# Performance work log

Hardware: AMD Instinct MI355X
Metric: run time of the kernel (lower is better)

The kernel has to match this reference:

```python
import jax, jax.numpy as jnp
import numpy as np

NUM_BRANCHES = 3
NUM_LAYERS = 4
HIDDEN = 256
IN_DIM = 128
NUM_GRAPHS = 256
NUM_CLASSES = 10
TOPK_RATIO = 0.5
GATE_INIT = 0.8


def matrix_neighbors(branch, layer, num_branches):
    nbrs = []
    if layer > 0:
        nbrs.append((branch, layer - 1))
    for other in (branch - 1, branch + 1):
        if 0 <= other < num_branches:
            nbrs.append((other, layer))
    if layer > 0:
        for other in (branch - 1, branch + 1):
            if 0 <= other < num_branches:
                nbrs.append((other, layer - 1))
    return nbrs


def topk_mask(t, ratio):
    d = t.shape[-1]
    k = max(1, min(d, int(np.ceil(d * ratio))))
    if k >= d:
        return jnp.ones_like(t)
    _, idx = jax.lax.top_k(jnp.abs(t), k)
    rows = jnp.arange(t.shape[0])[:, None]
    return jnp.zeros_like(t).at[rows, idx].set(1.0)


def setup_inputs():
    key = jax.random.key(0)
    ks = jax.random.split(key, 10)
    n, e = 50000, 800000
    x = jax.random.normal(ks[0], (n, IN_DIM), dtype=jnp.float32)
    edge_index = jax.random.randint(ks[1], (2, e), 0, n)
    batch = jnp.sort(jax.random.randint(ks[2], (n,), 0, NUM_GRAPHS))
    s = 0.05
    Win = jax.random.normal(ks[3], (NUM_BRANCHES, IN_DIM, HIDDEN), dtype=jnp.float32) * s
    b_in = jnp.zeros((NUM_BRANCHES, HIDDEN), dtype=jnp.float32)
    Whid = jax.random.normal(ks[4], (NUM_LAYERS - 1, NUM_BRANCHES, HIDDEN, HIDDEN), dtype=jnp.float32) * s
    bhid = jnp.zeros((NUM_LAYERS - 1, NUM_BRANCHES, HIDDEN), dtype=jnp.float32)
    gate_logit = jnp.asarray(np.log(GATE_INIT / (1.0 - GATE_INIT)), dtype=jnp.float32)
    Wc = jax.random.normal(ks[5], (HIDDEN, NUM_CLASSES), dtype=jnp.float32) * s
    bc = jnp.zeros((NUM_CLASSES,), dtype=jnp.float32)
    return {"x": x, "edge_index": edge_index, "batch": batch, "Win": Win,
            "b_in": b_in, "Whid": Whid, "bhid": bhid, "gate_logit": gate_logit,
            "Wc": Wc, "bc": bc}


def _forward(x, edge_index, batch, Win, b_in, Whid, bhid, gate_logit, Wc, bc):
    n = x.shape[0]
    loops = jnp.arange(n)
    row = jnp.concatenate([edge_index[0], loops])  # source
    col = jnp.concatenate([edge_index[1], loops])  # target
    deg = jax.ops.segment_sum(jnp.ones_like(col, dtype=x.dtype), col, num_segments=n)
    dinv = jnp.where(deg > 0, jax.lax.rsqrt(deg), 0.0)
    norm = dinv[row] * dinv[col]  # [E+N]

    def gcn(h, W, b):
        hw = h @ W  # [n, H]
        agg = jax.ops.segment_sum(hw[row] * norm[:, None], col, num_segments=n)
        return agg + b

    gate = jax.nn.sigmoid(gate_logit)
    states = [x for _ in range(NUM_BRANCHES)]
    for layer in range(NUM_LAYERS):
        props = []
        for b in range(NUM_BRANCHES):
            if layer == 0:
                p = gcn(states[b], Win[b], b_in[b])
            else:
                p = gcn(states[b], Whid[layer - 1, b], bhid[layer - 1, b])
            props.append(jax.nn.relu(p))
        new_states = []
        for b in range(NUM_BRANCHES):
            fused = props[b]
            nbrs = matrix_neighbors(b, layer, NUM_BRANCHES)
            if nbrs:
                rs = jnp.zeros_like(fused)
                for (sb, sl) in nbrs:
                    src = props[sb] if sl == layer else states[sb]
                    rs = rs + src * topk_mask(src, TOPK_RATIO)
                fused = fused + gate * rs
            new_states.append(jax.nn.relu(fused))  # dropout is identity in eval
        states = new_states

    counts = jax.ops.segment_sum(jnp.ones((n,), dtype=x.dtype), batch, num_segments=NUM_GRAPHS)
    denom = jnp.maximum(counts, 1.0)[:, None]
    embs = [jax.ops.segment_sum(s, batch, num_segments=NUM_GRAPHS) / denom for s in states]
    final = jnp.mean(jnp.stack(embs, axis=0), axis=0)  # [G, H]
    logits = final @ Wc + bc
    return logits, final


def reference(x, edge_index, batch, Win, b_in, Whid, bhid, gate_logit, Wc, bc):
    return _forward(x, edge_index, batch, Win, b_in, Whid, bhid, gate_logit, Wc, bc)
```

## Files before the change

kernel.cpp:

```cpp
#include <hip/hip_runtime.h>
#include <hip/hip_fp16.h>

#define NB 3
#define HIDDEN 256
#define INDIM 128
#define NGRAPH 256
#define NCLS 10
#define NMAX 50048
#define EMAX 800000

typedef unsigned short u16;
typedef unsigned long long ull;
typedef _Float16 f16_t;
typedef f16_t f16x8 __attribute__((ext_vector_type(8)));
typedef float f32x4 __attribute__((ext_vector_type(4)));

__device__ __align__(16) u16   g_states[(size_t)NMAX * NB * HIDDEN];
__device__ __align__(16) u16   g_props [(size_t)NMAX * NB * HIDDEN];
__device__ __align__(16) u16   g_agg3 [(size_t)NMAX * NB * HIDDEN];
__device__ __align__(16) u16   g_xh    [(size_t)NMAX * INDIM];
__device__ __align__(16) u16   g_whin [(size_t)NB * INDIM * HIDDEN];
__device__ __align__(16) u16   g_whid [(size_t)9 * HIDDEN * HIDDEN];
__device__ float g_fin   [NGRAPH * HIDDEN];
__device__ float g_dinv  [NMAX];
__device__ float g_ewts  [EMAX];
__device__ int   g_rowptr[NMAX + 1];
__device__ int   g_cidx  [EMAX];
__device__ int   g_cnt   [NMAX];
__device__ int   g_gs    [NGRAPH];
__device__ int   g_gc    [NGRAPH];

union HU { u16 u; __half h; };
__device__ __forceinline__ float h2f(u16 v) { HU x; x.u = v; return __half2float(x.h); }
__device__ __forceinline__ u16 f2h(float f) { HU x; x.h = __float2half_rn(f); return x.u; }
__device__ __forceinline__ float relu_f(float x) { return x > 0.f ? x : 0.f; }

__device__ __forceinline__ void fma8(float* acc, uint4 v, float w) {
    unsigned uu[4] = {v.x, v.y, v.z, v.w};
    #pragma unroll
    for (int q = 0; q < 4; ++q) {
        HU lo, hi; lo.u = (u16)(uu[q] & 0xFFFFu); hi.u = (u16)(uu[q] >> 16);
        acc[q * 2 + 0] += w * __half2float(lo.h);
        acc[q * 2 + 1] += w * __half2float(hi.h);
    }
}

__global__ void zero_cnt_k(int n) {
    int i = blockIdx.x * 256 + threadIdx.x;
    if (i < n) g_cnt[i] = 0;
}
__global__ void zero_gk() {
    int i = threadIdx.x;
    g_gs[i] = 0; g_gc[i] = 0;
}
__global__ void cvt_xh_k(const float* __restrict__ x, int cnt) {
    int i = blockIdx.x * 256 + threadIdx.x;
    if (i < cnt) g_xh[i] = f2h(x[i]);
}
__global__ void cvt_wt_k(const float* __restrict__ src, int which, int K, int total) {
    int i = blockIdx.x * 256 + threadIdx.x;
    if (i >= total) return;
    int kc = K * 256;
    int b = i / kc; int rem = i - b * kc;
    int k = rem >> 8; int c = rem & 255;
    u16* dst = which ? g_whid : g_whin;
    dst[(size_t)b * kc + (size_t)c * K + k] = f2h(src[i]);
}

__global__ void count_edges_k(const int* __restrict__ col, int E) {
    int i = blockIdx.x * 256 + threadIdx.x;
    if (i < E) atomicAdd(&g_cnt[col[i]], 1);
}
__global__ void dinv_k(int n) {
    int i = blockIdx.x * 256 + threadIdx.x;
    if (i < n) g_dinv[i] = rsqrtf((float)(g_cnt[i] + 1));
}
__global__ __launch_bounds__(1024) void scan_k(int n) {
    __shared__ int sm[1024];
    __shared__ int carry_s;
    int t = threadIdx.x;
    if (t == 0) carry_s = 0;
    __syncthreads();
    for (int base = 0; base < n; base += 1024) {
        int i = base + t;
        int v = (i < n) ? g_cnt[i] : 0;
        sm[t] = v;
        __syncthreads();
        for (int off = 1; off < 1024; off <<= 1) {
            int u = (t >= off) ? sm[t - off] : 0;
            __syncthreads();
            sm[t] += u;
            __syncthreads();
        }
        int incl = sm[t];
        int c0 = carry_s;
        if (i < n) g_rowptr[i] = c0 + incl - v;
        __syncthreads();
        if (t == 0) carry_s += sm[1023];
        __syncthreads();
    }
    if (t == 0) g_rowptr[n] = carry_s;
}
__global__ void fill_csr_k(const int* __restrict__ row, const int* __restrict__ col, int E) {
    int i = blockIdx.x * 256 + threadIdx.x;
    if (i >= E) return;
    int r = row[i], c = col[i];
    int pos = g_rowptr[c] + atomicAdd(&g_cnt[c], 1);
    g_cidx[pos] = r;
    g_ewts[pos] = g_dinv[r] * g_dinv[c];
}

__global__ __launch_bounds__(256) void agg256x3_k(int n) {
    int node = blockIdx.x * 4 + (threadIdx.x >> 6);
    if (node >= n) return;
    int lane = threadIdx.x & 63;
    int half = lane >> 5;
    int li   = lane & 31;
    const uint4* Sv = (const uint4*)g_states;
    float acc0[8] = {0,0,0,0,0,0,0,0}, acc1[8] = {0,0,0,0,0,0,0,0}, acc2[8] = {0,0,0,0,0,0,0,0};
    int e0 = g_rowptr[node], deg = g_rowptr[node + 1] - e0;
    int m = deg + 1;
    int j = half;
    if (half == 0) {
        float di = g_dinv[node];
        float w0 = di * di;
        size_t base = (size_t)node * 96 + li;
        fma8(acc0, Sv[base], w0);
        fma8(acc1, Sv[base + 32], w0);
        fma8(acc2, Sv[base + 64], w0);
        j = 2;
    }
    #pragma unroll 2
    for (; j < m; j += 2) {
        int s = g_cidx[e0 + j - 1];
        float w = g_ewts[e0 + j - 1];
        size_t base = (size_t)s * 96 + li;
        uint4 v0 = Sv[base], v1 = Sv[base + 32], v2 = Sv[base + 64];
        fma8(acc0, v0, w); fma8(acc1, v1, w); fma8(acc2, v2, w);
    }
    #pragma unroll
    for (int q = 0; q < 8; ++q) {
        acc0[q] += __shfl_xor(acc0[q], 32);
        acc1[q] += __shfl_xor(acc1[q], 32);
        acc2[q] += __shfl_xor(acc2[q], 32);
    }
    if (half == 0) {
        uint4* Av = (uint4*)g_agg3;
        size_t base = (size_t)node * 96 + li;
        uint4 o;
        unsigned* ou = (unsigned*)&o;
        #pragma unroll
        for (int q = 0; q < 4; ++q) ou[q] = (unsigned)f2h(acc0[q*2]) | ((unsigned)f2h(acc0[q*2+1]) << 16);
        Av[base] = o;
        #pragma unroll
        for (int q = 0; q < 4; ++q) ou[q] = (unsigned)f2h(acc1[q*2]) | ((unsigned)f2h(acc1[q*2+1]) << 16);
        Av[base + 32] = o;
        #pragma unroll
        for (int q = 0; q < 4; ++q) ou[q] = (unsigned)f2h(acc2[q*2]) | ((unsigned)f2h(acc2[q*2+1]) << 16);
        Av[base + 64] = o;
    }
}

__global__ __launch_bounds__(256) void agg128_k(int n) {
    int node = blockIdx.x * 4 + (threadIdx.x >> 6);
    if (node >= n) return;
    int lane = threadIdx.x & 63;
    int grp = lane >> 4;
    int li  = lane & 15;
    const uint4* Xv = (const uint4*)g_xh;
    float acc[8] = {0,0,0,0,0,0,0,0};
    int e0 = g_rowptr[node], deg = g_rowptr[node + 1] - e0;
    int m = deg + 1;
    int j = grp;
    if (grp == 0) {
        float di = g_dinv[node];
        fma8(acc, Xv[(size_t)node * 16 + li], di * di);
        j = 4;
    }
    #pragma unroll 2
    for (; j < m; j += 4) {
        int s = g_cidx[e0 + j - 1];
        float w = g_ewts[e0 + j - 1];
        fma8(acc, Xv[(size_t)s * 16 + li], w);
    }
    #pragma unroll
    for (int q = 0; q < 8; ++q) {
        acc[q] += __shfl_xor(acc[q], 16);
        acc[q] += __shfl_xor(acc[q], 32);
    }
    if (grp == 0) {
        uint4 o; unsigned* ou = (unsigned*)&o;
        #pragma unroll
        for (int q = 0; q < 4; ++q) ou[q] = (unsigned)f2h(acc[q*2]) | ((unsigned)f2h(acc[q*2+1]) << 16);
        ((uint4*)g_agg3)[(size_t)node * 16 + li] = o;
    }
}

template<int K>
__global__ __launch_bounds__(256) void gemm_mfma_k(int wsel, int rowStride, int brMul,
        const float* __restrict__ bias0, int n) {
    int br = blockIdx.y;
    const f16_t* A  = (const f16_t*)g_agg3 + (size_t)br * brMul;
    const f16_t* Wt = (wsel < 0) ? (const f16_t*)g_whin + (size_t)br * K * 256
                                 : (const f16_t*)g_whid + (size_t)(wsel + br) * K * 256;
    const float* bias = bias0 + (size_t)br * 256;
    u16* C = g_props + (size_t)br * 256;
    int t = threadIdx.x, l = t & 63, w = t >> 6;
    int row0 = blockIdx.x * 64;
    int c0 = w * 64;
    int mrow = l & 15;
    int kg = (l >> 4) * 8;
    f32x4 acc[4][4];
    #pragma unroll
    for (int rt = 0; rt < 4; ++rt)
        #pragma unroll
        for (int ct = 0; ct < 4; ++ct) acc[rt][ct] = (f32x4){0.f, 0.f, 0.f, 0.f};

    for (int k0 = 0; k0 < K; k0 += 32) {
        f16x8 af[4], bf[4];
        #pragma unroll
        for (int rt = 0; rt < 4; ++rt) {
            int r = row0 + rt * 16 + mrow;
            af[rt] = *(const f16x8*)(A + (size_t)r * rowStride + k0 + kg);
        }
        #pragma unroll
        for (int ct = 0; ct < 4; ++ct) {
            int c = c0 + ct * 16 + mrow;
            bf[ct] = *(const f16x8*)(Wt + (size_t)c * K + k0 + kg);
        }
        #pragma unroll
        for (int rt = 0; rt < 4; ++rt)
            #pragma unroll
            for (int ct = 0; ct < 4; ++ct)
                acc[rt][ct] = __builtin_amdgcn_mfma_f32_16x16x32_f16(af[rt], bf[ct], acc[rt][ct], 0, 0, 0);
    }
    int rb = (l >> 4) * 4;
    #pragma unroll
    for (int ct = 0; ct < 4; ++ct) {
        int c = c0 + ct * 16 + mrow;
        float bv = bias[c];
        #pragma unroll
        for (int rt = 0; rt < 4; ++rt) {
            #pragma unroll
            for (int q = 0; q < 4; ++q) {
                int r = row0 + rt * 16 + rb + q;
                if (r < n) C[(size_t)r * 768 + c] = f2h(relu_f(acc[rt][ct][q] + bv));
            }
        }
    }
}

template<int CNT>
__device__ __forceinline__ void topk_multi(const ushort4* hu, const float4* v, float4* out) {
    int lane = threadIdx.x & 63;
    unsigned lo[CNT], hi[CNT]; int cge[CNT];
    #pragma unroll
    for (int s = 0; s < CNT; ++s) { lo[s] = 0; hi[s] = 0x7BFF; cge[s] = 256; }
    for (int it = 0; it < 15; ++it) {
        #pragma unroll
        for (int s = 0; s < CNT; ++s) {
            unsigned mid = (lo[s] + hi[s] + 1) >> 1;
            int c = __popcll(__ballot(hu[s].x >= mid)) + __popcll(__ballot(hu[s].y >= mid))
                  + __popcll(__ballot(hu[s].z >= mid)) + __popcll(__ballot(hu[s].w >= mid));
            if (c >= 128) { lo[s] = mid; cge[s] = c; } else hi[s] = mid - 1;
        }
    }
    #pragma unroll
    for (int s = 0; s < CNT; ++s) {
        unsigned thr = lo[s];
        unsigned a0 = hu[s].x, a1 = hu[s].y, a2 = hu[s].z, a3 = hu[s].w;
        float4 r;
        if (cge[s] == 128) {
            r.x = (a0 >= thr) ? v[s].x : 0.f;
            r.y = (a1 >= thr) ? v[s].y : 0.f;
            r.z = (a2 >= thr) ? v[s].z : 0.f;
            r.w = (a3 >= thr) ? v[s].w : 0.f;
        } else {
            ull b0 = __ballot(a0 == thr), b1 = __ballot(a1 == thr);
            ull b2 = __ballot(a2 == thr), b3 = __ballot(a3 == thr);
            int cgt = __popcll(__ballot(a0 > thr)) + __popcll(__ballot(a1 > thr))
                    + __popcll(__ballot(a2 > thr)) + __popcll(__ballot(a3 > thr));
            int need = 128 - cgt;
            ull below = (lane == 0) ? 0ull : (~0ull >> (64 - lane));
            int base = __popcll(b0 & below) + __popcll(b1 & below)
                     + __popcll(b2 & below) + __popcll(b3 & below);
            int o0 = (int)((b0 >> lane) & 1), o1 = (int)((b1 >> lane) & 1), o2 = (int)((b2 >> lane) & 1);
            int p0 = base, p1 = base + o0, p2 = p1 + o1, p3 = p2 + o2;
            r.x = (a0 > thr || (a0 == thr && p0 < need)) ? v[s].x : 0.f;
            r.y = (a1 > thr || (a1 == thr && p1 < need)) ? v[s].y : 0.f;
            r.z = (a2 > thr || (a2 == thr && p2 < need)) ? v[s].z : 0.f;
            r.w = (a3 > thr || (a3 == thr && p3 < need)) ? v[s].w : 0.f;
        }
        out[s] = r;
    }
}

__device__ __forceinline__ float4 dec4(ushort4 h) {
    float4 r; r.x = h2f(h.x); r.y = h2f(h.y); r.z = h2f(h.z); r.w = h2f(h.w);
    return r;
}
__device__ __forceinline__ void st4h(u16* p, size_t off, float4 v) {
    ushort4 o; o.x = f2h(v.x); o.y = f2h(v.y); o.z = f2h(v.z); o.w = f2h(v.w);
    ((ushort4*)p)[off] = o;
}

__global__ __launch_bounds__(256) void fuse0_k(const float* __restrict__ gate_logit, int n) {
    int node = blockIdx.x * 4 + (threadIdx.x >> 6);
    if (node >= n) return;
    int lane = threadIdx.x & 63;
    size_t base4 = (size_t)node * 192 + lane;
    float g = 1.f / (1.f + expf(-gate_logit[0]));
    const ushort4* P = (const ushort4*)g_props;
    ushort4 hu[3]; float4 v[3], m[3];
    hu[0] = P[base4]; hu[1] = P[base4 + 64]; hu[2] = P[base4 + 128];
    v[0] = dec4(hu[0]); v[1] = dec4(hu[1]); v[2] = dec4(hu[2]);
    topk_multi<3>(hu, v, m);
    float4 o0, o1, o2;
    o0.x = relu_f(v[0].x + g * m[1].x); o0.y = relu_f(v[0].y + g * m[1].y);
    o0.z = relu_f(v[0].z + g * m[1].z); o0.w = relu_f(v[0].w + g * m[1].w);
    o1.x = relu_f(v[1].x + g * (m[0].x + m[2].x)); o1.y = relu_f(v[1].y + g * (m[0].y + m[2].y));
    o1.z = relu_f(v[1].z + g * (m[0].z + m[2].z)); o1.w = relu_f(v[1].w + g * (m[0].w + m[2].w));
    o2.x = relu_f(v[2].x + g * m[1].x); o2.y = relu_f(v[2].y + g * m[1].y);
    o2.z = relu_f(v[2].z + g * m[1].z); o2.w = relu_f(v[2].w + g * m[1].w);
    st4h(g_states, base4, o0); st4h(g_states, base4 + 64, o1); st4h(g_states, base4 + 128, o2);
}

__global__ __launch_bounds__(256) void fuse_k(const float* __restrict__ gate_logit, int n) {
    int node = blockIdx.x * 4 + (threadIdx.x >> 6);
    if (node >= n) return;
    int lane = threadIdx.x & 63;
    size_t base4 = (size_t)node * 192 + lane;
    float g = 1.f / (1.f + expf(-gate_logit[0]));
    const ushort4* P = (const ushort4*)g_props;
    const ushort4* S = (const ushort4*)g_states;
    ushort4 hu[6]; float4 v[6], m[6];
    hu[0] = P[base4]; hu[1] = P[base4 + 64]; hu[2] = P[base4 + 128];
    hu[3] = S[base4]; hu[4] = S[base4 + 64]; hu[5] = S[base4 + 128];
    #pragma unroll
    for (int s = 0; s < 6; ++s) v[s] = dec4(hu[s]);
    topk_multi<6>(hu, v, m);
    float4 o0, o1, o2;
    o0.x = relu_f(v[0].x + g * (m[3].x + m[1].x + m[4].x));
    o0.y = relu_f(v[0].y + g * (m[3].y + m[1].y + m[4].y));
    o0.z = relu_f(v[0].z + g * (m[3].z + m[1].z + m[4].z));
    o0.w = relu_f(v[0].w + g * (m[3].w + m[1].w + m[4].w));
    o1.x = relu_f(v[1].x + g * (m[4].x + m[0].x + m[3].x + m[2].x + m[5].x));
    o1.y = relu_f(v[1].y + g * (m[4].y + m[0].y + m[3].y + m[2].y + m[5].y));
    o1.z = relu_f(v[1].z + g * (m[4].z + m[0].z + m[3].z + m[2].z + m[5].z));
    o1.w = relu_f(v[1].w + g * (m[4].w + m[0].w + m[3].w + m[2].w + m[5].w));
    o2.x = relu_f(v[2].x + g * (m[5].x + m[1].x + m[4].x));
    o2.y = relu_f(v[2].y + g * (m[5].y + m[1].y + m[4].y));
    o2.z = relu_f(v[2].z + g * (m[5].z + m[1].z + m[4].z));
    o2.w = relu_f(v[2].w + g * (m[5].w + m[1].w + m[4].w));
    st4h(g_states, base4, o0); st4h(g_states, base4 + 64, o1); st4h(g_states, base4 + 128, o2);
}

__global__ void gbounds_k(const int* __restrict__ batch, int n) {
    int i = blockIdx.x * 256 + threadIdx.x;
    if (i >= n) return;
    int g = batch[i];
    atomicAdd(&g_gc[g], 1);
    if (i == 0 || batch[i - 1] != g) g_gs[g] = i;
}

__global__ __launch_bounds__(256) void greduce_k(float* __restrict__ outfin, int n) {
    int g = blockIdx.x, d = threadIdx.x;
    int st = g_gs[g], c = g_gc[g];
    float a = 0.f;
    for (int i = st; i < st + c; ++i) {
        size_t o = (size_t)i * 768 + d;
        a += h2f(g_states[o]) + h2f(g_states[o + 256]) + h2f(g_states[o + 512]);
    }
    float r = a / (3.0f * (float)(c > 0 ? c : 1));
    g_fin[g * 256 + d] = r;
    outfin[(size_t)g * 256 + d] = r;
}

__global__ void logits_k(const float* __restrict__ Wc, const float* __restrict__ bc,
                         float* __restrict__ out) {
    int idx = blockIdx.x * 256 + threadIdx.x;
    if (idx >= NGRAPH * NCLS) return;
    int g = idx / NCLS, c = idx % NCLS;
    float s = bc[c];
    for (int k = 0; k < 256; ++k) s += g_fin[g * 256 + k] * Wc[k * NCLS + c];
    out[idx] = s;
}

extern "C" void kernel_launch(void* const* d_in, const int* in_sizes, int n_in,
                              void* d_out, int out_size, void* d_ws, size_t ws_size,
                              hipStream_t stream) {
    const float* x       = (const float*)d_in[0];
    const int*   eidx    = (const int*)d_in[1];
    const int*   batch   = (const int*)d_in[2];
    const float* Win     = (const float*)d_in[3];
    const float* b_in    = (const float*)d_in[4];
    const float* Whid    = (const float*)d_in[5];
    const float* bhid    = (const float*)d_in[6];
    const float* gate_l  = (const float*)d_in[7];
    const float* Wc      = (const float*)d_in[8];
    const float* bc      = (const float*)d_in[9];
    float* out = (float*)d_out;

    const int n = in_sizes[0] / INDIM;
    const int E = in_sizes[1] / 2;
    if (n > NMAX || E > EMAX) return;
    const int* erow = eidx;
    const int* ecol = eidx + E;

    float* outfin = out + NGRAPH * NCLS;

    const int TB = 256;
    dim3 b256(TB);
    int nblkN = (n + TB - 1) / TB;
    int eblk  = (E + TB - 1) / TB;
    int nblk4 = (n + 3) / 4;
    dim3 ggrid((n + 63) / 64, NB);

    zero_cnt_k<<<nblkN, b256, 0, stream>>>(n);
    cvt_xh_k<<<(n * INDIM + TB - 1) / TB, b256, 0, stream>>>(x, n * INDIM);
    cvt_wt_k<<<(NB * INDIM * HIDDEN + TB - 1) / TB, b256, 0, stream>>>(Win, 0, INDIM, NB * INDIM * HIDDEN);
    cvt_wt_k<<<(9 * HIDDEN * HIDDEN + TB - 1) / TB, b256, 0, stream>>>(Whid, 1, HIDDEN, 9 * HIDDEN * HIDDEN);
    count_edges_k<<<eblk, b256, 0, stream>>>(ecol, E);
    dinv_k<<<nblkN, b256, 0, stream>>>(n);
    scan_k<<<1, 1024, 0, stream>>>(n);
    zero_cnt_k<<<nblkN, b256, 0, stream>>>(n);
    fill_csr_k<<<eblk, b256, 0, stream>>>(erow, ecol, E);

    agg128_k<<<nblk4, b256, 0, stream>>>(n);
    gemm_mfma_k<INDIM><<<ggrid, b256, 0, stream>>>(-1, INDIM, 0, b_in, n);
    fuse0_k<<<nblk4, b256, 0, stream>>>(gate_l, n);

    for (int l = 1; l < 4; ++l) {
        agg256x3_k<<<nblk4, b256, 0, stream>>>(n);
        gemm_mfma_k<HIDDEN><<<ggrid, b256, 0, stream>>>((l - 1) * NB, NB * HIDDEN, HIDDEN,
                bhid + (size_t)(l - 1) * NB * HIDDEN, n);
        fuse_k<<<nblk4, b256, 0, stream>>>(gate_l, n);
    }

    zero_gk<<<1, 256, 0, stream>>>();
    gbounds_k<<<nblkN, b256, 0, stream>>>(batch, n);
    greduce_k<<<NGRAPH, b256, 0, stream>>>(outfin, n);
    logits_k<<<(NGRAPH * NCLS + TB - 1) / TB, b256, 0, stream>>>(Wc, bc, out);
}
```

Before: 1.869 ms.

## Parallelize CSR scan, tile weight transpose, vectorize input conversion and graph reduce

Replaces the single-block serial prefix scan over node degrees with a three-kernel multi-block scan using block sums. Converts weights with a shared-memory tiled transpose so both the reads and the writes are coalesced. Vectorizes the x-to-half conversion with float4 loads and makes the per-graph reduction read ushort4 across all three branches. Together these target preprocessing and tail overheads, at the cost of two extra kernel launches.

```diff
diff --git a/kernel.cpp b/kernel.cpp
--- a/kernel.cpp
+++ b/kernel.cpp
@@ -27,6 +27,7 @@
 __device__ int   g_rowptr[NMAX + 1];
 __device__ int   g_cidx  [EMAX];
 __device__ int   g_cnt   [NMAX];
+__device__ int   g_bsum  [64];
 __device__ int   g_gs    [NGRAPH];
 __device__ int   g_gc    [NGRAPH];
 
@@ -53,18 +54,32 @@
     int i = threadIdx.x;
     g_gs[i] = 0; g_gc[i] = 0;
 }
-__global__ void cvt_xh_k(const float* __restrict__ x, int cnt) {
-    int i = blockIdx.x * 256 + threadIdx.x;
-    if (i < cnt) g_xh[i] = f2h(x[i]);
-}
-__global__ void cvt_wt_k(const float* __restrict__ src, int which, int K, int total) {
-    int i = blockIdx.x * 256 + threadIdx.x;
-    if (i >= total) return;
-    int kc = K * 256;
-    int b = i / kc; int rem = i - b * kc;
-    int k = rem >> 8; int c = rem & 255;
-    u16* dst = which ? g_whid : g_whin;
-    dst[(size_t)b * kc + (size_t)c * K + k] = f2h(src[i]);
+__global__ void cvt_xh_k(const float* __restrict__ x, int cnt4) {
+    int i = blockIdx.x * 256 + threadIdx.x;
+    if (i >= cnt4) return;
+    float4 v = ((const float4*)x)[i];
+    ushort4 o; o.x = f2h(v.x); o.y = f2h(v.y); o.z = f2h(v.z); o.w = f2h(v.w);
+    ((ushort4*)g_xh)[i] = o;
+}
+__global__ void cvt_wt_k(const float* __restrict__ src, int which, int K) {
+    __shared__ u16 tile[32][33];
+    int k0 = blockIdx.x * 32, c0 = blockIdx.y * 32, b = blockIdx.z;
+    int t = threadIdx.x;
+    int tc = t & 31, tk = t >> 5;
+    const float* S = src + (size_t)b * K * 256;
+    #pragma unroll
+    for (int q = 0; q < 4; ++q) {
+        int kk = tk * 4 + q;
+        tile[kk][tc] = f2h(S[(size_t)(k0 + kk) * 256 + c0 + tc]);
+    }
+    __syncthreads();
+    u16* D = (which ? g_whid : g_whin) + (size_t)b * K * 256;
+    int kx = t & 31, cg = t >> 5;
+    #pragma unroll
+    for (int q = 0; q < 4; ++q) {
+        int c = c0 + cg * 4 + q;
+        D[(size_t)c * K + k0 + kx] = tile[kx][cg * 4 + q];
+    }
 }
 
 __global__ void count_edges_k(const int* __restrict__ col, int E) {
@@ -75,31 +90,38 @@
     int i = blockIdx.x * 256 + threadIdx.x;
     if (i < n) g_dinv[i] = rsqrtf((float)(g_cnt[i] + 1));
 }
-__global__ __launch_bounds__(1024) void scan_k(int n) {
+__global__ __launch_bounds__(1024) void scan1_k(int n) {
     __shared__ int sm[1024];
-    __shared__ int carry_s;
+    int blk = blockIdx.x, t = threadIdx.x;
+    int i = blk * 1024 + t;
+    int v = (i < n) ? g_cnt[i] : 0;
+    sm[t] = v;
+    __syncthreads();
+    for (int off = 1; off < 1024; off <<= 1) {
+        int u = (t >= off) ? sm[t - off] : 0;
+        __syncthreads();
+        sm[t] += u;
+        __syncthreads();
+    }
+    if (i < n) g_rowptr[i + 1] = sm[t];
+    if (t == 1023) g_bsum[blk] = sm[t];
+    if (blk == 0 && t == 0) g_rowptr[0] = 0;
+}
+__global__ void scan2_k(int nblk) {
     int t = threadIdx.x;
-    if (t == 0) carry_s = 0;
-    __syncthreads();
-    for (int base = 0; base < n; base += 1024) {
-        int i = base + t;
-        int v = (i < n) ? g_cnt[i] : 0;
-        sm[t] = v;
-        __syncthreads();
-        for (int off = 1; off < 1024; off <<= 1) {
-            int u = (t >= off) ? sm[t - off] : 0;
-            __syncthreads();
-            sm[t] += u;
-            __syncthreads();
-        }
-        int incl = sm[t];
-        int c0 = carry_s;
-        if (i < n) g_rowptr[i] = c0 + incl - v;
-        __syncthreads();
-        if (t == 0) carry_s += sm[1023];
-        __syncthreads();
-    }
-    if (t == 0) g_rowptr[n] = carry_s;
+    int v = (t < nblk) ? g_bsum[t] : 0;
+    #pragma unroll
+    for (int off = 1; off < 64; off <<= 1) {
+        int u = __shfl_up(v, off);
+        if (t >= off) v += u;
+    }
+    if (t < nblk) g_bsum[t] = v;
+}
+__global__ void scan3_k(int n) {
+    int i = blockIdx.x * 256 + threadIdx.x;
+    if (i >= n) return;
+    int blk = i >> 10;
+    if (blk > 0) g_rowptr[i + 1] += g_bsum[blk - 1];
 }
 __global__ void fill_csr_k(const int* __restrict__ row, const int* __restrict__ col, int E) {
     int i = blockIdx.x * 256 + threadIdx.x;
@@ -364,16 +386,23 @@
 }
 
 __global__ __launch_bounds__(256) void greduce_k(float* __restrict__ outfin, int n) {
-    int g = blockIdx.x, d = threadIdx.x;
+    __shared__ float sums[768];
+    int g = blockIdx.x, t = threadIdx.x;
     int st = g_gs[g], c = g_gc[g];
-    float a = 0.f;
-    for (int i = st; i < st + c; ++i) {
-        size_t o = (size_t)i * 768 + d;
-        a += h2f(g_states[o]) + h2f(g_states[o + 256]) + h2f(g_states[o + 512]);
-    }
-    float r = a / (3.0f * (float)(c > 0 ? c : 1));
-    g_fin[g * 256 + d] = r;
-    outfin[(size_t)g * 256 + d] = r;
+    if (t < 192) {
+        const ushort4* S = (const ushort4*)g_states;
+        float a0 = 0.f, a1 = 0.f, a2 = 0.f, a3 = 0.f;
+        for (int i = st; i < st + c; ++i) {
+            ushort4 v = S[(size_t)i * 192 + t];
+            a0 += h2f(v.x); a1 += h2f(v.y); a2 += h2f(v.z); a3 += h2f(v.w);
+        }
+        sums[t * 4 + 0] = a0; sums[t * 4 + 1] = a1;
+        sums[t * 4 + 2] = a2; sums[t * 4 + 3] = a3;
+    }
+    __syncthreads();
+    float r = (sums[t] + sums[256 + t] + sums[512 + t]) / (3.0f * (float)(c > 0 ? c : 1));
+    g_fin[g * 256 + t] = r;
+    outfin[(size_t)g * 256 + t] = r;
 }
 
 __global__ void logits_k(const float* __restrict__ Wc, const float* __restrict__ bc,
@@ -414,15 +443,20 @@
     int nblkN = (n + TB - 1) / TB;
     int eblk  = (E + TB - 1) / TB;
     int nblk4 = (n + 3) / 4;
+    int sblk  = (n + 1023) / 1024;
     dim3 ggrid((n + 63) / 64, NB);
+    dim3 wgin(INDIM / 32, HIDDEN / 32, NB);
+    dim3 wghid(HIDDEN / 32, HIDDEN / 32, 9);
 
     zero_cnt_k<<<nblkN, b256, 0, stream>>>(n);
-    cvt_xh_k<<<(n * INDIM + TB - 1) / TB, b256, 0, stream>>>(x, n * INDIM);
-    cvt_wt_k<<<(NB * INDIM * HIDDEN + TB - 1) / TB, b256, 0, stream>>>(Win, 0, INDIM, NB * INDIM * HIDDEN);
-    cvt_wt_k<<<(9 * HIDDEN * HIDDEN + TB - 1) / TB, b256, 0, stream>>>(Whid, 1, HIDDEN, 9 * HIDDEN * HIDDEN);
+    cvt_xh_k<<<(n * INDIM / 4 + TB - 1) / TB, b256, 0, stream>>>(x, n * INDIM / 4);
+    cvt_wt_k<<<wgin, b256, 0, stream>>>(Win, 0, INDIM);
+    cvt_wt_k<<<wghid, b256, 0, stream>>>(Whid, 1, HIDDEN);
     count_edges_k<<<eblk, b256, 0, stream>>>(ecol, E);
     dinv_k<<<nblkN, b256, 0, stream>>>(n);
-    scan_k<<<1, 1024, 0, stream>>>(n);
+    scan1_k<<<sblk, 1024, 0, stream>>>(n);
+    scan2_k<<<1, 64, 0, stream>>>(sblk);
+    scan3_k<<<nblkN, b256, 0, stream>>>(n);
     zero_cnt_k<<<nblkN, b256, 0, stream>>>(n);
     fill_csr_k<<<eblk, b256, 0, stream>>>(erow, ecol, E);
 
```

After: 1.766 ms. -5.5%, faster.
